# Kernel optimization log

Measured on AMD Instinct MI355X. Metric: run time of the kernel, lower is better.

Reference implementation:

```python
import jax, jax.numpy as jnp
import numpy as np

DIM_SINGLE = 384
DIM_PAIR = 128
HEADS = 12
DIM_POINT = 4
B, N = 1, 1024
EPS = 1e-5


def _gram_schmidt_rot(key, shape):
    k1, k2 = jax.random.split(key)
    v1 = jax.random.normal(k1, shape + (3,), jnp.float32)
    v2 = jax.random.normal(k2, shape + (3,), jnp.float32)
    x = v1 / jnp.linalg.norm(v1, axis=-1, keepdims=True)
    z = jnp.cross(x, v2)
    z = z / jnp.linalg.norm(z, axis=-1, keepdims=True)
    y = jnp.cross(z, x)
    # columns are basis vectors, matching torch.stack([x,y,z], dim=-1)
    return jnp.stack([x, y, z], axis=-1)


def setup_inputs() -> dict:
    key = jax.random.key(0)
    ks = jax.random.split(key, 24)
    C, Cp, H, P = DIM_SINGLE, DIM_PAIR, HEADS, DIM_POINT
    HP3 = H * P * 3
    s = lambda k, sh, sc: (jax.random.normal(k, sh, jnp.float32) * sc)
    inp = {
        'single': jax.random.normal(ks[0], (B, N, C), jnp.float32),
        'pair': jax.random.normal(ks[1], (B, N, N, Cp), jnp.float32),
        'rot': _gram_schmidt_rot(ks[2], (B, N)),
        'trans': jax.random.normal(ks[3], (B, N, 3), jnp.float32),
        'mask': jnp.ones((B, N), dtype=bool),
        'Wq': s(ks[4], (C, C), C ** -0.5), 'bq': jnp.zeros((C,), jnp.float32),
        'Wk': s(ks[5], (C, C), C ** -0.5), 'bk': jnp.zeros((C,), jnp.float32),
        'Wv': s(ks[6], (C, C), C ** -0.5), 'bv': jnp.zeros((C,), jnp.float32),
        'Wpb': s(ks[7], (Cp, H), Cp ** -0.5), 'bpb': jnp.zeros((H,), jnp.float32),
        'Wqp': s(ks[8], (C, HP3), C ** -0.5), 'bqp': jnp.zeros((HP3,), jnp.float32),
        'Wkp': s(ks[9], (C, HP3), C ** -0.5), 'bkp': jnp.zeros((HP3,), jnp.float32),
        'Wvp': s(ks[10], (C, HP3), C ** -0.5), 'bvp': jnp.zeros((HP3,), jnp.float32),
        'Wo': s(ks[11], (C, C), C ** -0.5), 'bo': jnp.zeros((C,), jnp.float32),
        'Wpo': s(ks[12], (HP3, C), HP3 ** -0.5), 'bpo': jnp.zeros((C,), jnp.float32),
        'gamma': jnp.ones((C,), jnp.float32), 'beta': jnp.zeros((C,), jnp.float32),
    }
    return inp


def ipa_forward(single, pair, rot, trans, mask,
                Wq, bq, Wk, bk, Wv, bv, Wpb, bpb,
                Wqp, bqp, Wkp, bkp, Wvp, bvp,
                Wo, bo, Wpo, bpo, gamma, beta):
    Bn, Nn, C = single.shape
    H, P = HEADS, DIM_POINT
    Ch = C // H
    scale = Ch ** -0.5

    q = (single @ Wq + bq).reshape(Bn, Nn, H, Ch)
    k = (single @ Wk + bk).reshape(Bn, Nn, H, Ch)
    v = (single @ Wv + bv).reshape(Bn, Nn, H, Ch)

    pair_bias = (pair @ Wpb + bpb).transpose(0, 3, 1, 2)  # [B,H,N,N]

    def pts(W, b):
        p = (single @ W + b).reshape(Bn, Nn, H, P, 3)
        # point as row-vector times rot (matches torch einsum bnhpd,bnhde->bnhpe)
        p = jnp.einsum('bnhpd,bnde->bnhpe', p, rot) + trans[:, :, None, None, :]
        return p

    q_pts = pts(Wqp, bqp)
    k_pts = pts(Wkp, bkp)
    v_pts = pts(Wvp, bvp)

    q2 = jnp.sum(q_pts ** 2, axis=(3, 4))  # [B,N,H]
    k2 = jnp.sum(k_pts ** 2, axis=(3, 4))

    scalar_logits = jnp.einsum('bmhc,bnhc->bhmn', q, k) * scale
    qk_pts = jnp.einsum('bmhpd,bnhpd->bhmn', q_pts, k_pts)
    point_logits = -0.5 * (q2.transpose(0, 2, 1)[:, :, :, None]
                           + k2.transpose(0, 2, 1)[:, :, None, :]
                           - 2.0 * qk_pts) * scale
    logits = scalar_logits + point_logits + pair_bias

    mask2d = mask[:, None, :, None] & mask[:, None, None, :]  # [B,1,M,N]
    logits = jnp.where(mask2d, logits, -1e9)

    attn = jax.nn.softmax(logits, axis=-1)  # [B,H,M,N]

    out_scalar = jnp.einsum('bhmn,bnhc->bmhc', attn, v).reshape(Bn, Nn, C)
    out_points = jnp.einsum('bhmn,bnhpd->bmhpd', attn, v_pts).reshape(Bn, Nn, H * P * 3)

    out = out_scalar @ Wo + bo + out_points @ Wpo + bpo
    x = single + out
    mu = jnp.mean(x, axis=-1, keepdims=True)
    var = jnp.var(x, axis=-1, keepdims=True)
    return (x - mu) / jnp.sqrt(var + EPS) * gamma + beta


def reference(single, pair, rot, trans, mask,
              Wq, bq, Wk, bk, Wv, bv, Wpb, bpb,
              Wqp, bqp, Wkp, bkp, Wvp, bvp,
              Wo, bo, Wpo, bpo, gamma, beta):
    return ipa_forward(single, pair, rot, trans, mask,
                       Wq, bq, Wk, bk, Wv, bv, Wpb, bpb,
                       Wqp, bqp, Wkp, bkp, Wvp, bvp,
                       Wo, bo, Wpo, bpo, gamma, beta)
```

## Files before the change

### kernel.cpp

```cpp
#include <hip/hip_runtime.h>
#include <cmath>


#define SCALE 0.17677669529663687f

#define OFF_QQ 0u
#define OFF_KK 589824u
#define OFF_VV 1179648u
#define OFF_SM 1769472u
#define OFF_SIS 1781760u
#define OFF_OA4 1794048u
#define OFF_OA 3956736u
#define OFF_LG 4497408u
#define OFF_PM 17080320u
#define OFF_PS 17178624u
#define WS_FLOATS 17276928ull

__device__ __forceinline__ void fma4(float4& a, const float4& w, float s) {
  a.x = fmaf(w.x, s, a.x); a.y = fmaf(w.y, s, a.y);
  a.z = fmaf(w.z, s, a.z); a.w = fmaf(w.w, s, a.w);
}

__global__ __launch_bounds__(256) void k_gemm(
    const float* __restrict__ single, const float* __restrict__ rotm,
    const float* __restrict__ trans, const float* __restrict__ bpb,
    const float* __restrict__ Wq, const float* __restrict__ bq,
    const float* __restrict__ Wk, const float* __restrict__ bk,
    const float* __restrict__ Wv, const float* __restrict__ bv,
    const float* __restrict__ Wqp, const float* __restrict__ bqp,
    const float* __restrict__ Wkp, const float* __restrict__ bkp,
    const float* __restrict__ Wvp, const float* __restrict__ bvp,
    float* __restrict__ ws)
{
  __shared__ float sA[64 * 37];
  __shared__ float sB[48 * 37];
  const int tid = threadIdx.x;
  const int m0 = blockIdx.x * 64;
  const int ct = blockIdx.y;
  float* QQ = ws + OFF_QQ; float* KK = ws + OFF_KK; float* VV = ws + OFF_VV;
  const float* W; const float* bb; int OUT, cb, w_;
  if (ct < 24) {
    w_ = ct >> 3;
    W  = w_ == 0 ? Wq : (w_ == 1 ? Wk : Wv);
    bb = w_ == 0 ? bq : (w_ == 1 ? bk : bv);
    OUT = 384; cb = (ct & 7) * 48;
  } else {
    int pt = ct - 24; w_ = pt / 3;
    W  = w_ == 0 ? Wqp : (w_ == 1 ? Wkp : Wvp);
    bb = w_ == 0 ? bqp : (w_ == 1 ? bkp : bvp);
    OUT = 144; cb = (pt - w_ * 3) * 48;
  }
  const int tr = tid >> 4, tc = tid & 15;
  const int r0 = tr * 4;
  const int k4s = tid & 7, mrs = tid >> 3;
  const int c4b = tid % 12, kkb = tid / 12;
  const int f1 = tid + 256;
  const int c4b1 = f1 % 12, kkb1 = f1 / 12;

  float acc[4][3];
  #pragma unroll
  for (int i = 0; i < 4; ++i)
    #pragma unroll
    for (int j = 0; j < 3; ++j) acc[i][j] = 0.f;

  float4 pa0 = *(const float4*)&single[(size_t)(m0 + mrs) * 384 + k4s * 4];
  float4 pa1 = *(const float4*)&single[(size_t)(m0 + mrs + 32) * 384 + k4s * 4];
  float4 pb0 = *(const float4*)&W[(size_t)kkb * OUT + cb + c4b * 4];
  float4 pb1;
  if (tid < 128) pb1 = *(const float4*)&W[(size_t)kkb1 * OUT + cb + c4b1 * 4];

  for (int kc = 0; kc < 12; ++kc) {
    *(float4*)&sA[mrs * 37 + k4s * 4] = pa0;
    *(float4*)&sA[(mrs + 32) * 37 + k4s * 4] = pa1;
    sB[(c4b * 4 + 0) * 37 + kkb] = pb0.x;
    sB[(c4b * 4 + 1) * 37 + kkb] = pb0.y;
    sB[(c4b * 4 + 2) * 37 + kkb] = pb0.z;
    sB[(c4b * 4 + 3) * 37 + kkb] = pb0.w;
    if (tid < 128) {
      sB[(c4b1 * 4 + 0) * 37 + kkb1] = pb1.x;
      sB[(c4b1 * 4 + 1) * 37 + kkb1] = pb1.y;
      sB[(c4b1 * 4 + 2) * 37 + kkb1] = pb1.z;
      sB[(c4b1 * 4 + 3) * 37 + kkb1] = pb1.w;
    }
    if (kc < 11) {
      int kn = (kc + 1) * 32;
      pa0 = *(const float4*)&single[(size_t)(m0 + mrs) * 384 + kn + k4s * 4];
      pa1 = *(const float4*)&single[(size_t)(m0 + mrs + 32) * 384 + kn + k4s * 4];
      pb0 = *(const float4*)&W[(size_t)(kn + kkb) * OUT + cb + c4b * 4];
      if (tid < 128) pb1 = *(const float4*)&W[(size_t)(kn + kkb1) * OUT + cb + c4b1 * 4];
    }
    __syncthreads();
    #pragma unroll
    for (int k4 = 0; k4 < 8; ++k4) {
      float4 av[4], bv_[3];
      #pragma unroll
      for (int i = 0; i < 4; ++i) av[i] = *(const float4*)&sA[(r0 + i) * 37 + k4 * 4];
      #pragma unroll
      for (int j = 0; j < 3; ++j) bv_[j] = *(const float4*)&sB[(tc * 3 + j) * 37 + k4 * 4];
      #pragma unroll
      for (int i = 0; i < 4; ++i)
        #pragma unroll
        for (int j = 0; j < 3; ++j)
          acc[i][j] += av[i].x * bv_[j].x + av[i].y * bv_[j].y
                     + av[i].z * bv_[j].z + av[i].w * bv_[j].w;
    }
    __syncthreads();
  }

  if (ct < 24) {
    #pragma unroll
    for (int i = 0; i < 4; ++i) {
      int m = m0 + r0 + i;
      #pragma unroll
      for (int j = 0; j < 3; ++j) {
        int c = cb + tc * 3 + j;
        float v = acc[i][j] + bb[c];
        int h = c >> 5, cc = c & 31;
        if (w_ == 0)      QQ[h * 49152 + m * 48 + cc] = SCALE * v;
        else if (w_ == 1) KK[h * 49152 + m * 48 + cc] = v;
        else              VV[m * 576 + h * 48 + cc] = v;
      }
    }
  } else {
    const int pe = cb / 3 + tc;
    const int h = pe >> 2, p = pe & 3;
    #pragma unroll
    for (int i = 0; i < 4; ++i) {
      int m = m0 + r0 + i;
      const float* R = rotm + m * 9;
      float raw0 = acc[i][0] + bb[cb + tc * 3 + 0];
      float raw1 = acc[i][1] + bb[cb + tc * 3 + 1];
      float raw2 = acc[i][2] + bb[cb + tc * 3 + 2];
      float v0 = raw0 * R[0] + raw1 * R[3] + raw2 * R[6] + trans[m * 3 + 0];
      float v1 = raw0 * R[1] + raw1 * R[4] + raw2 * R[7] + trans[m * 3 + 1];
      float v2 = raw0 * R[2] + raw1 * R[5] + raw2 * R[8] + trans[m * 3 + 2];
      if (w_ == 2) {
        float* d = VV + m * 576 + h * 48 + 32 + p * 3;
        d[0] = v0; d[1] = v1; d[2] = v2;
      } else {
        float s2 = v0 * v0 + v1 * v1 + v2 * v2;
        s2 += __shfl_xor(s2, 1);
        s2 += __shfl_xor(s2, 2);
        if (w_ == 0) {
          float* d = QQ + h * 49152 + m * 48;
          d[32 + p * 3 + 0] = SCALE * v0;
          d[32 + p * 3 + 1] = SCALE * v1;
          d[32 + p * 3 + 2] = SCALE * v2;
          if (p == 0) {
            d[44] = 1.f; d[45] = -0.5f * SCALE * s2; d[46] = 0.f; d[47] = 0.f;
          }
        } else {
          float* d = KK + h * 49152 + m * 48;
          d[32 + p * 3 + 0] = v0;
          d[32 + p * 3 + 1] = v1;
          d[32 + p * 3 + 2] = v2;
          if (p == 0) {
            d[44] = bpb[h] - 0.5f * SCALE * s2; d[45] = 1.f;
            d[46] = 0.f; d[47] = 0.f;
          }
        }
      }
    }
  }
}

__global__ __launch_bounds__(256) void k_qkdot(const float* __restrict__ QQ,
                                               const float* __restrict__ KK,
                                               float* __restrict__ LG)
{
  __shared__ float sQ[64 * 52];
  __shared__ float sK[128 * 52];
  const int tid = threadIdx.x;
  const int n0 = blockIdx.x * 128, m0 = blockIdx.y * 64, hh = blockIdx.z;
  const float* Qg = QQ + (size_t)hh * 49152 + (size_t)m0 * 48;
  const float* Kg = KK + (size_t)hh * 49152 + (size_t)n0 * 48;
  for (int i = tid; i < 768; i += 256) {
    int r = i / 12, c4 = (i - r * 12) * 4;
    *(float4*)&sQ[r * 52 + c4] = *(const float4*)&Qg[r * 48 + c4];
  }
  for (int i = tid; i < 1536; i += 256) {
    int r = i / 12, c4 = (i - r * 12) * 4;
    *(float4*)&sK[r * 52 + c4] = *(const float4*)&Kg[r * 48 + c4];
  }
  __syncthreads();
  const int mb = (tid >> 4) * 4, nb = tid & 15;
  float acc[4][8];
  #pragma unroll
  for (int i = 0; i < 4; ++i)
    #pragma unroll
    for (int j = 0; j < 8; ++j) acc[i][j] = 0.f;
  #pragma unroll
  for (int j4 = 0; j4 < 48; j4 += 4) {
    float4 q[4], k[8];
    #pragma unroll
    for (int i = 0; i < 4; ++i) q[i] = *(const float4*)&sQ[(mb + i) * 52 + j4];
    #pragma unroll
    for (int j = 0; j < 8; ++j) k[j] = *(const float4*)&sK[(nb + j * 16) * 52 + j4];
    #pragma unroll
    for (int i = 0; i < 4; ++i)
      #pragma unroll
      for (int j = 0; j < 8; ++j)
        acc[i][j] += q[i].x * k[j].x + q[i].y * k[j].y + q[i].z * k[j].z + q[i].w * k[j].w;
  }
  float* Lb = LG + (size_t)hh * 1048576 + (size_t)m0 * 1024 + n0;
  #pragma unroll
  for (int i = 0; i < 4; ++i)
    #pragma unroll
    for (int j = 0; j < 8; ++j)
      Lb[(mb + i) * 1024 + nb + j * 16] = acc[i][j];
}

__global__ __launch_bounds__(128) void k_bias(const float* __restrict__ pair,
                                              const float* __restrict__ Wpb,
                                              float* __restrict__ LG,
                                              float* __restrict__ PM,
                                              float* __restrict__ PS)
{
  __shared__ float sP[128 * 33];
  __shared__ float sRed[2][12];
  __shared__ float sRed2[2][12];
  const int tid = threadIdx.x;
  const size_t base = (size_t)blockIdx.x * 128;
  const int c4 = tid & 7, r8 = tid >> 3;
  float acc[12];
  #pragma unroll
  for (int h = 0; h < 12; ++h) acc[h] = 0.f;

  float4 pre[8];
  #pragma unroll
  for (int k = 0; k < 8; ++k)
    pre[k] = *(const float4*)&pair[(base + k * 16 + r8) * 128 + c4 * 4];

  for (int cc = 0; cc < 4; ++cc) {
    #pragma unroll
    for (int k = 0; k < 8; ++k) {
      float* d = &sP[(k * 16 + r8) * 33 + c4 * 4];
      d[0] = pre[k].x; d[1] = pre[k].y; d[2] = pre[k].z; d[3] = pre[k].w;
    }
    if (cc < 3) {
      #pragma unroll
      for (int k = 0; k < 8; ++k)
        pre[k] = *(const float4*)&pair[(base + k * 16 + r8) * 128 + (cc + 1) * 32 + c4 * 4];
    }
    __syncthreads();
    const float* rp = &sP[tid * 33];
    #pragma unroll 8
    for (int j = 0; j < 32; ++j) {
      float p = rp[j];
      const float* w = Wpb + (cc * 32 + j) * 12;
      #pragma unroll
      for (int h = 0; h < 12; ++h) acc[h] = fmaf(p, w[h], acc[h]);
    }
    __syncthreads();
  }
  float lf[12];
  float* L = LG + base + tid;
  #pragma unroll
  for (int h = 0; h < 12; ++h) {
    lf[h] = L[(size_t)h * 1048576] + acc[h];
    L[(size_t)h * 1048576] = lf[h];
  }
  const int lane = tid & 63, wv = tid >> 6;
  #pragma unroll
  for (int h = 0; h < 12; ++h) {
    float mx = lf[h];
    #pragma unroll
    for (int d = 32; d; d >>= 1) mx = fmaxf(mx, __shfl_xor(mx, d));
    if (lane == 0) sRed[wv][h] = mx;
  }
  __syncthreads();
  float Mq[12];
  #pragma unroll
  for (int h = 0; h < 12; ++h)
    Mq[h] = fmaxf(sRed[0][h], sRed[1][h]);
  #pragma unroll
  for (int h = 0; h < 12; ++h) {
    float se = __expf(lf[h] - Mq[h]);
    #pragma unroll
    for (int d = 32; d; d >>= 1) se += __shfl_xor(se, d);
    if (lane == 0) sRed2[wv][h] = se;
  }
  __syncthreads();
  if (tid < 12) {
    float S = sRed2[0][tid] + sRed2[1][tid];
    int m = blockIdx.x >> 3, q = blockIdx.x & 7;
    PM[tid * 8192 + m * 8 + q] = Mq[tid];
    PS[tid * 8192 + m * 8 + q] = S;
  }
}

__global__ __launch_bounds__(256) void k_mstats(const float* __restrict__ PM,
                                                const float* __restrict__ PS,
                                                float* __restrict__ SM,
                                                float* __restrict__ SIS)
{
  int idx = blockIdx.x * 256 + threadIdx.x;
  if (idx >= 12288) return;
  int b = idx * 8;
  float M = -3.0e38f;
  #pragma unroll
  for (int i = 0; i < 8; ++i) M = fmaxf(M, PM[b + i]);
  float S = 0.f;
  #pragma unroll
  for (int i = 0; i < 8; ++i) S += PS[b + i] * __expf(PM[b + i] - M);
  SM[idx] = M;
  SIS[idx] = 1.f / S;
}

__global__ __launch_bounds__(256) void k_av(const float* __restrict__ LG,
                                            const float* __restrict__ VV,
                                            const float* __restrict__ SM,
                                            float* __restrict__ OA4)
{
  __shared__ float sA[64 * 68];
  __shared__ float sBt[48 * 68];
  __shared__ float sMl[64];
  const int tid = threadIdx.x;
  const int m0 = blockIdx.x * 64, n0 = blockIdx.y * 256, hh = blockIdx.z;
  const int q = blockIdx.y;
  const float* Lh = LG + (size_t)hh * 1048576;
  const int mi4 = tid >> 4, cj3 = tid & 15;

  if (tid < 64) sMl[tid] = SM[hh * 1024 + m0 + tid];
  for (int i = tid; i < 4 * 68; i += 256) sBt[44 * 68 + i] = 0.f;
  __syncthreads();

  float acc[4][3];
  #pragma unroll
  for (int i = 0; i < 4; ++i)
    #pragma unroll
    for (int j = 0; j < 3; ++j) acc[i][j] = 0.f;

  for (int kc = 0; kc < 4; ++kc) {
    const int nb = n0 + kc * 64;
    #pragma unroll
    for (int t = 0; t < 4; ++t) {
      int idx = tid + t * 256;
      int row = idx >> 4, c4 = idx & 15;
      float4 x = *(const float4*)&Lh[(size_t)(m0 + row) * 1024 + nb + c4 * 4];
      float mrow = sMl[row];
      float4 e;
      e.x = __expf(x.x - mrow); e.y = __expf(x.y - mrow);
      e.z = __expf(x.z - mrow); e.w = __expf(x.w - mrow);
      *(float4*)&sA[row * 68 + c4 * 4] = e;
    }
    for (int idx = tid; idx < 704; idx += 256) {
      int r = idx / 11, c4 = idx - r * 11;
      float4 v = *(const float4*)&VV[(size_t)(nb + r) * 576 + hh * 48 + c4 * 4];
      sBt[(c4 * 4 + 0) * 68 + r] = v.x;
      sBt[(c4 * 4 + 1) * 68 + r] = v.y;
      sBt[(c4 * 4 + 2) * 68 + r] = v.z;
      sBt[(c4 * 4 + 3) * 68 + r] = v.w;
    }
    __syncthreads();
    #pragma unroll 4
    for (int k4 = 0; k4 < 16; ++k4) {
      float4 a0 = *(const float4*)&sA[(mi4 * 4 + 0) * 68 + k4 * 4];
      float4 a1 = *(const float4*)&sA[(mi4 * 4 + 1) * 68 + k4 * 4];
      float4 a2 = *(const float4*)&sA[(mi4 * 4 + 2) * 68 + k4 * 4];
      float4 a3 = *(const float4*)&sA[(mi4 * 4 + 3) * 68 + k4 * 4];
      float4 b0 = *(const float4*)&sBt[(cj3 * 3 + 0) * 68 + k4 * 4];
      float4 b1 = *(const float4*)&sBt[(cj3 * 3 + 1) * 68 + k4 * 4];
      float4 b2 = *(const float4*)&sBt[(cj3 * 3 + 2) * 68 + k4 * 4];
      acc[0][0] += a0.x*b0.x + a0.y*b0.y + a0.z*b0.z + a0.w*b0.w;
      acc[0][1] += a0.x*b1.x + a0.y*b1.y + a0.z*b1.z + a0.w*b1.w;
      acc[0][2] += a0.x*b2.x + a0.y*b2.y + a0.z*b2.z + a0.w*b2.w;
      acc[1][0] += a1.x*b0.x + a1.y*b0.y + a1.z*b0.z + a1.w*b0.w;
      acc[1][1] += a1.x*b1.x + a1.y*b1.y + a1.z*b1.z + a1.w*b1.w;
      acc[1][2] += a1.x*b2.x + a1.y*b2.y + a1.z*b2.z + a1.w*b2.w;
      acc[2][0] += a2.x*b0.x + a2.y*b0.y + a2.z*b0.z + a2.w*b0.w;
      acc[2][1] += a2.x*b1.x + a2.y*b1.y + a2.z*b1.z + a2.w*b1.w;
      acc[2][2] += a2.x*b2.x + a2.y*b2.y + a2.z*b2.z + a2.w*b2.w;
      acc[3][0] += a3.x*b0.x + a3.y*b0.y + a3.z*b0.z + a3.w*b0.w;
      acc[3][1] += a3.x*b1.x + a3.y*b1.y + a3.z*b1.z + a3.w*b1.w;
      acc[3][2] += a3.x*b2.x + a3.y*b2.y + a3.z*b2.z + a3.w*b2.w;
    }
    __syncthreads();
  }
  #pragma unroll
  for (int i = 0; i < 4; ++i)
    #pragma unroll
    for (int j = 0; j < 3; ++j) {
      int c = cj3 * 3 + j;
      if (c < 44)
        OA4[(size_t)q * 540672 + (size_t)(m0 + mi4 * 4 + i) * 528 + hh * 44 + c]
            = acc[i][j];
    }
}

__global__ __launch_bounds__(256) void k_merge(const float* __restrict__ OA4,
                                               const float* __restrict__ SIS,
                                               float* __restrict__ OA)
{
  int idx = blockIdx.x * 256 + threadIdx.x;
  if (idx >= 540672) return;
  int m = idx / 528, c = idx - m * 528;
  int h = c / 44;
  float v = OA4[idx] + OA4[540672 + idx] + OA4[2 * 540672 + idx]
          + OA4[3 * 540672 + idx];
  OA[idx] = v * SIS[h * 1024 + m];
}

__global__ __launch_bounds__(128) void k_final(
    const float* __restrict__ OA, const float* __restrict__ single,
    const float* __restrict__ Wo, const float* __restrict__ bo,
    const float* __restrict__ Wpo, const float* __restrict__ bpo,
    const float* __restrict__ gamma, const float* __restrict__ beta,
    float* __restrict__ out)
{
  __shared__ float sX[2 * 384];
  const int tid = threadIdx.x;
  const int m0 = blockIdx.x * 2;
  if (tid < 96) {
    int o4 = tid * 4;
    float4 b1 = *(const float4*)&bo[o4];
    float4 b2 = *(const float4*)&bpo[o4];
    float4 bs = make_float4(b1.x + b2.x, b1.y + b2.y, b1.z + b2.z, b1.w + b2.w);
    float4 acc[2] = {bs, bs};
    const float* oab = OA + (size_t)m0 * 528;
    #pragma unroll 1
    for (int hh = 0; hh < 12; ++hh) {
      #pragma unroll
      for (int j4 = 0; j4 < 8; ++j4) {
        const float* wp = Wo + (size_t)(hh * 32 + j4 * 4) * 384 + o4;
        float4 w0 = *(const float4*)(wp);
        float4 w1 = *(const float4*)(wp + 384);
        float4 w2 = *(const float4*)(wp + 768);
        float4 w3 = *(const float4*)(wp + 1152);
        #pragma unroll
        for (int mi = 0; mi < 2; ++mi) {
          float4 s = *(const float4*)(oab + mi * 528 + hh * 44 + j4 * 4);
          fma4(acc[mi], w0, s.x); fma4(acc[mi], w1, s.y);
          fma4(acc[mi], w2, s.z); fma4(acc[mi], w3, s.w);
        }
      }
      #pragma unroll
      for (int j4 = 0; j4 < 3; ++j4) {
        const float* wp = Wpo + (size_t)(hh * 12 + j4 * 4) * 384 + o4;
        float4 w0 = *(const float4*)(wp);
        float4 w1 = *(const float4*)(wp + 384);
        float4 w2 = *(const float4*)(wp + 768);
        float4 w3 = *(const float4*)(wp + 1152);
        #pragma unroll
        for (int mi = 0; mi < 2; ++mi) {
          float4 s = *(const float4*)(oab + mi * 528 + hh * 44 + 32 + j4 * 4);
          fma4(acc[mi], w0, s.x); fma4(acc[mi], w1, s.y);
          fma4(acc[mi], w2, s.z); fma4(acc[mi], w3, s.w);
        }
      }
    }
    #pragma unroll
    for (int mi = 0; mi < 2; ++mi) {
      float4 sg = *(const float4*)&single[(size_t)(m0 + mi) * 384 + o4];
      float4 x = make_float4(acc[mi].x + sg.x, acc[mi].y + sg.y,
                             acc[mi].z + sg.z, acc[mi].w + sg.w);
      *(float4*)&sX[mi * 384 + o4] = x;
    }
  }
  __syncthreads();
  const int lane = tid & 63, r = tid >> 6;
  float xs[6]; float s = 0.f;
  #pragma unroll
  for (int i = 0; i < 6; ++i) { xs[i] = sX[r * 384 + lane * 6 + i]; s += xs[i]; }
  #pragma unroll
  for (int d = 32; d; d >>= 1) s += __shfl_xor(s, d);
  float mu = s * (1.f / 384.f);
  float vs = 0.f;
  #pragma unroll
  for (int i = 0; i < 6; ++i) { float dd = xs[i] - mu; vs = fmaf(dd, dd, vs); }
  #pragma unroll
  for (int d = 32; d; d >>= 1) vs += __shfl_xor(vs, d);
  float rstd = rsqrtf(vs * (1.f / 384.f) + 1e-5f);
  #pragma unroll
  for (int i = 0; i < 6; ++i) {
    int c = lane * 6 + i;
    out[(size_t)(m0 + r) * 384 + c] = (xs[i] - mu) * rstd * gamma[c] + beta[c];
  }
}

__global__ void k_wsfail(float* out, int n) {
  int i = blockIdx.x * 256 + threadIdx.x;
  if (i < n) out[i] = 12345.0f;
}

extern "C" void kernel_launch(void* const* d_in, const int* in_sizes, int n_in,
                              void* d_out, int out_size, void* d_ws, size_t ws_size,
                              hipStream_t stream)
{
  (void)in_sizes; (void)n_in;
  const float* single = (const float*)d_in[0];
  const float* pair   = (const float*)d_in[1];
  const float* rotm   = (const float*)d_in[2];
  const float* trans  = (const float*)d_in[3];
  const float* Wq  = (const float*)d_in[5];
  const float* bq  = (const float*)d_in[6];
  const float* Wk  = (const float*)d_in[7];
  const float* bk  = (const float*)d_in[8];
  const float* Wv  = (const float*)d_in[9];
  const float* bv  = (const float*)d_in[10];
  const float* Wpb = (const float*)d_in[11];
  const float* bpb = (const float*)d_in[12];
  const float* Wqp = (const float*)d_in[13];
  const float* bqp = (const float*)d_in[14];
  const float* Wkp = (const float*)d_in[15];
  const float* bkp = (const float*)d_in[16];
  const float* Wvp = (const float*)d_in[17];
  const float* bvp = (const float*)d_in[18];
  const float* Wo  = (const float*)d_in[19];
  const float* bo  = (const float*)d_in[20];
  const float* Wpo = (const float*)d_in[21];
  const float* bpo = (const float*)d_in[22];
  const float* gamma = (const float*)d_in[23];
  const float* beta  = (const float*)d_in[24];
  float* ws  = (float*)d_ws;
  float* out = (float*)d_out;

  if (ws_size < WS_FLOATS * 4ull) {
    k_wsfail<<<(out_size + 255) / 256, 256, 0, stream>>>(out, out_size);
    return;
  }

  k_gemm<<<dim3(16, 33), 256, 0, stream>>>(single, rotm, trans, bpb,
      Wq, bq, Wk, bk, Wv, bv, Wqp, bqp, Wkp, bkp, Wvp, bvp, ws);
  k_qkdot<<<dim3(8, 16, 12), 256, 0, stream>>>(ws + OFF_QQ, ws + OFF_KK,
                                               ws + OFF_LG);
  k_bias<<<8192, 128, 0, stream>>>(pair, Wpb, ws + OFF_LG, ws + OFF_PM,
                                   ws + OFF_PS);
  k_mstats<<<48, 256, 0, stream>>>(ws + OFF_PM, ws + OFF_PS, ws + OFF_SM,
                                   ws + OFF_SIS);
  k_av<<<dim3(16, 4, 12), 256, 0, stream>>>(ws + OFF_LG, ws + OFF_VV,
                                            ws + OFF_SM, ws + OFF_OA4);
  k_merge<<<2112, 256, 0, stream>>>(ws + OFF_OA4, ws + OFF_SIS, ws + OFF_OA);
  k_final<<<512, 128, 0, stream>>>(ws + OFF_OA, single, Wo, bo, Wpo, bpo,
                                   gamma, beta, out);
}
```

Before: 310.9 us.

## Fold softmax stats and partial-sum merge into AV and final kernels

Removes the separate k_mstats and k_merge launches. k_av now computes each row's max from the partial maxima, and k_final computes the inverse softmax normaliser, sums the four split-N partial outputs into shared memory, then runs the output projection from shared memory. This drops two kernel launches and the global write and read of the merged OA buffer, at the cost of some redundant max and exp work in every block.

```diff
diff --git a/kernel.cpp b/kernel.cpp
--- a/kernel.cpp
+++ b/kernel.cpp
@@ -7,10 +7,7 @@
 #define OFF_QQ 0u
 #define OFF_KK 589824u
 #define OFF_VV 1179648u
-#define OFF_SM 1769472u
-#define OFF_SIS 1781760u
 #define OFF_OA4 1794048u
-#define OFF_OA 3956736u
 #define OFF_LG 4497408u
 #define OFF_PM 17080320u
 #define OFF_PS 17178624u
@@ -289,27 +286,9 @@
   }
 }
 
-__global__ __launch_bounds__(256) void k_mstats(const float* __restrict__ PM,
-                                                const float* __restrict__ PS,
-                                                float* __restrict__ SM,
-                                                float* __restrict__ SIS)
-{
-  int idx = blockIdx.x * 256 + threadIdx.x;
-  if (idx >= 12288) return;
-  int b = idx * 8;
-  float M = -3.0e38f;
-  #pragma unroll
-  for (int i = 0; i < 8; ++i) M = fmaxf(M, PM[b + i]);
-  float S = 0.f;
-  #pragma unroll
-  for (int i = 0; i < 8; ++i) S += PS[b + i] * __expf(PM[b + i] - M);
-  SM[idx] = M;
-  SIS[idx] = 1.f / S;
-}
-
 __global__ __launch_bounds__(256) void k_av(const float* __restrict__ LG,
                                             const float* __restrict__ VV,
-                                            const float* __restrict__ SM,
+                                            const float* __restrict__ PM,
                                             float* __restrict__ OA4)
 {
   __shared__ float sA[64 * 68];
@@ -321,7 +300,13 @@
   const float* Lh = LG + (size_t)hh * 1048576;
   const int mi4 = tid >> 4, cj3 = tid & 15;
 
-  if (tid < 64) sMl[tid] = SM[hh * 1024 + m0 + tid];
+  if (tid < 64) {
+    const float* pm = PM + hh * 8192 + (m0 + tid) * 8;
+    float M = pm[0];
+    #pragma unroll
+    for (int i = 1; i < 8; ++i) M = fmaxf(M, pm[i]);
+    sMl[tid] = M;
+  }
   for (int i = tid; i < 4 * 68; i += 256) sBt[44 * 68 + i] = 0.f;
   __syncthreads();
 
@@ -388,36 +373,47 @@
     }
 }
 
-__global__ __launch_bounds__(256) void k_merge(const float* __restrict__ OA4,
-                                               const float* __restrict__ SIS,
-                                               float* __restrict__ OA)
-{
-  int idx = blockIdx.x * 256 + threadIdx.x;
-  if (idx >= 540672) return;
-  int m = idx / 528, c = idx - m * 528;
-  int h = c / 44;
-  float v = OA4[idx] + OA4[540672 + idx] + OA4[2 * 540672 + idx]
-          + OA4[3 * 540672 + idx];
-  OA[idx] = v * SIS[h * 1024 + m];
-}
-
 __global__ __launch_bounds__(128) void k_final(
-    const float* __restrict__ OA, const float* __restrict__ single,
+    const float* __restrict__ OA4, const float* __restrict__ PM,
+    const float* __restrict__ PS, const float* __restrict__ single,
     const float* __restrict__ Wo, const float* __restrict__ bo,
     const float* __restrict__ Wpo, const float* __restrict__ bpo,
     const float* __restrict__ gamma, const float* __restrict__ beta,
     float* __restrict__ out)
 {
   __shared__ float sX[2 * 384];
+  __shared__ float sOA[2 * 528];
+  __shared__ float sIS[2][12];
   const int tid = threadIdx.x;
   const int m0 = blockIdx.x * 2;
+  if (tid < 24) {
+    int m = tid / 12, h = tid - m * 12;
+    const float* pm = PM + h * 8192 + (m0 + m) * 8;
+    const float* ps = PS + h * 8192 + (m0 + m) * 8;
+    float M = pm[0];
+    #pragma unroll
+    for (int i = 1; i < 8; ++i) M = fmaxf(M, pm[i]);
+    float S = 0.f;
+    #pragma unroll
+    for (int i = 0; i < 8; ++i) S += ps[i] * __expf(pm[i] - M);
+    sIS[m][h] = 1.f / S;
+  }
+  __syncthreads();
+  for (int i = tid; i < 1056; i += 128) {
+    int m = i / 528, c = i - m * 528;
+    int h = c / 44;
+    size_t off = (size_t)(m0 + m) * 528 + c;
+    float v = OA4[off] + OA4[540672 + off] + OA4[2 * 540672 + off]
+            + OA4[3 * 540672 + off];
+    sOA[i] = v * sIS[m][h];
+  }
+  __syncthreads();
   if (tid < 96) {
     int o4 = tid * 4;
     float4 b1 = *(const float4*)&bo[o4];
     float4 b2 = *(const float4*)&bpo[o4];
     float4 bs = make_float4(b1.x + b2.x, b1.y + b2.y, b1.z + b2.z, b1.w + b2.w);
     float4 acc[2] = {bs, bs};
-    const float* oab = OA + (size_t)m0 * 528;
     #pragma unroll 1
     for (int hh = 0; hh < 12; ++hh) {
       #pragma unroll
@@ -429,7 +425,7 @@
         float4 w3 = *(const float4*)(wp + 1152);
         #pragma unroll
         for (int mi = 0; mi < 2; ++mi) {
-          float4 s = *(const float4*)(oab + mi * 528 + hh * 44 + j4 * 4);
+          float4 s = *(const float4*)&sOA[mi * 528 + hh * 44 + j4 * 4];
           fma4(acc[mi], w0, s.x); fma4(acc[mi], w1, s.y);
           fma4(acc[mi], w2, s.z); fma4(acc[mi], w3, s.w);
         }
@@ -443,7 +439,7 @@
         float4 w3 = *(const float4*)(wp + 1152);
         #pragma unroll
         for (int mi = 0; mi < 2; ++mi) {
-          float4 s = *(const float4*)(oab + mi * 528 + hh * 44 + 32 + j4 * 4);
+          float4 s = *(const float4*)&sOA[mi * 528 + hh * 44 + 32 + j4 * 4];
           fma4(acc[mi], w0, s.x); fma4(acc[mi], w1, s.y);
           fma4(acc[mi], w2, s.z); fma4(acc[mi], w3, s.w);
         }
@@ -526,11 +522,8 @@
                                                ws + OFF_LG);
   k_bias<<<8192, 128, 0, stream>>>(pair, Wpb, ws + OFF_LG, ws + OFF_PM,
                                    ws + OFF_PS);
-  k_mstats<<<48, 256, 0, stream>>>(ws + OFF_PM, ws + OFF_PS, ws + OFF_SM,
-                                   ws + OFF_SIS);
   k_av<<<dim3(16, 4, 12), 256, 0, stream>>>(ws + OFF_LG, ws + OFF_VV,
-                                            ws + OFF_SM, ws + OFF_OA4);
-  k_merge<<<2112, 256, 0, stream>>>(ws + OFF_OA4, ws + OFF_SIS, ws + OFF_OA);
-  k_final<<<512, 128, 0, stream>>>(ws + OFF_OA, single, Wo, bo, Wpo, bpo,
-                                   gamma, beta, out);
-}
+                                            ws + OFF_PM, ws + OFF_OA4);
+  k_final<<<512, 128, 0, stream>>>(ws + OFF_OA4, ws + OFF_PM, ws + OFF_PS,
+                                   single, Wo, bo, Wpo, bpo, gamma, beta, out);
+}
```

Result: slower. 346.9 us (+11.6%).
